# Kernel tuning notes

Hardware: AMD Instinct MI355X
Metric: run time of the kernel (lower is better)

Reference implementation:

```python
import jax, jax.numpy as jnp
import numpy as np

N_NODES = 200_000
N_EDGES = 6_400_000
N_GRAPHS = 512
F_IN = 92   # CGCNN atom feature dim
WIDTH = 10  # hard-coded config.width in GCNSimple
F_OUT = 1   # output_features


def setup_inputs() -> dict:
    key = jax.random.key(0)
    ks = jax.random.split(key, 10)
    atom_features = jax.random.normal(ks[0], (N_NODES, F_IN), dtype=jnp.float32)
    r = jax.random.normal(ks[1], (N_EDGES, 3), dtype=jnp.float32)
    W_emb = jax.random.normal(ks[2], (F_IN, WIDTH), dtype=jnp.float32) * 0.1
    b_emb = jax.random.normal(ks[3], (WIDTH,), dtype=jnp.float32) * 0.1
    W1 = jax.random.normal(ks[4], (WIDTH, WIDTH), dtype=jnp.float32) * 0.3
    b1 = jax.random.normal(ks[5], (WIDTH,), dtype=jnp.float32) * 0.1
    W2 = jax.random.normal(ks[6], (WIDTH, F_OUT), dtype=jnp.float32) * 0.3
    b2 = jax.random.normal(ks[7], (F_OUT,), dtype=jnp.float32) * 0.1
    src = jax.random.randint(ks[8], (N_EDGES,), 0, N_NODES, dtype=jnp.int32)
    dst = jax.random.randint(ks[9], (N_EDGES,), 0, N_NODES, dtype=jnp.int32)
    graph_ids = jnp.sort(jax.random.randint(jax.random.fold_in(key, 99), (N_NODES,), 0, N_GRAPHS, dtype=jnp.int32))
    return {
        "atom_features": atom_features, "r": r,
        "W_emb": W_emb, "b_emb": b_emb, "W1": W1, "b1": b1, "W2": W2, "b2": b2,
        "src": src, "dst": dst, "graph_ids": graph_ids, "num_graphs": N_GRAPHS,
    }


def reference(atom_features, r, W_emb, b_emb, W1, b1, W2, b2, src, dst, graph_ids, num_graphs):
    n = atom_features.shape[0]
    dt = atom_features.dtype
    # edge weights: exp(-||r||^2 / lengthscale^2), lengthscale = 1
    ew = jnp.exp(-jnp.sum(r * r, axis=1))  # [E]

    # unweighted degrees (DGL GraphConv norm='both' ignores edge_weight in norm)
    out_deg = jnp.clip(jnp.zeros(n, dt).at[src].add(1.0), 1.0)
    in_deg = jnp.clip(jnp.zeros(n, dt).at[dst].add(1.0), 1.0)
    inv_sqrt_out = out_deg ** -0.5
    inv_sqrt_in = in_deg ** -0.5

    def gconv(x, W, b, mm_first):
        # DGL GraphConv, norm='both': scale by src deg, weighted-sum aggregate,
        # scale by dst deg; weight applied before aggregation iff in > out.
        x = x * inv_sqrt_out[:, None]
        if mm_first:
            x = x @ W
        msg = x[src] * ew[:, None]                      # [E, d] gather
        agg = jax.ops.segment_sum(msg, dst, num_segments=n)  # [N, d] scatter-add
        if not mm_first:
            agg = agg @ W
        return agg * inv_sqrt_in[:, None] + b

    h = atom_features @ W_emb + b_emb                  # atom embedding [N, 10]
    x = jax.nn.relu(gconv(h, W1, b1, mm_first=False))  # 10 -> 10 (in == out: aggregate first)
    x = gconv(x, W2, b2, mm_first=True)                # 10 -> 1  (in > out: mm first)

    # AvgPooling: mean node feature per graph
    counts = jax.ops.segment_sum(jnp.ones(n, dt), graph_ids, num_segments=num_graphs)
    pooled = jax.ops.segment_sum(x, graph_ids, num_segments=num_graphs) / counts[:, None]
    return jnp.squeeze(pooled)  # [num_graphs]
```

## Files before the change

kernel.cpp:

```cpp
#include <hip/hip_runtime.h>
#include <math.h>

#define NNODES  200000
#define NEDGES  6400000
#define NGRAPHS 512
#define FIN     92
#define WID     10
#define HPAD    16
#define NBLK    ((NNODES + 255) / 256)

#define LBITS   10
#define LSIZE   1024
#define LMASK   (LSIZE - 1)
#define NB      196
#define PBLK    512
#define EPB     (NEDGES / PBLK)
#define TILE    2500
#define NTILE   (EPB / TILE)
#define CELLS   (2 * NB)
#define CNT_N   (CELLS * PBLK)
#define SBLKS   (CNT_N / 256)

#define CHBITS  14
#define NCHK    13
#define KEYS    (LSIZE * NCHK)
#define KPT     (KEYS / 256)

#define LPN     8
#define LPNSH   3
#define NPB     (256 / LPN)
#define AGG_BLKS (NNODES / NPB)

__global__ void k_part_count(const int* __restrict__ src,
                             const int* __restrict__ dst,
                             int* __restrict__ cnt) {
    __shared__ int hD[NB];
    __shared__ int hS[NB];
    int tid = threadIdx.x, k = blockIdx.x;
    if (tid < NB) { hD[tid] = 0; hS[tid] = 0; }
    __syncthreads();
    int base = k * EPB;
    for (int i = tid; i < EPB; i += 256) {
        int e = base + i;
        atomicAdd(&hD[dst[e] >> LBITS], 1);
        atomicAdd(&hS[src[e] >> LBITS], 1);
    }
    __syncthreads();
    if (tid < NB) {
        cnt[tid * PBLK + k] = hD[tid];
        cnt[(NB + tid) * PBLK + k] = hS[tid];
    }
}

__global__ void k_scan_partial(const int* __restrict__ cnt,
                               int* __restrict__ partial) {
    __shared__ int sdata[256];
    int tid = threadIdx.x;
    sdata[tid] = cnt[blockIdx.x * 256 + tid];
    __syncthreads();
    for (int s = 128; s > 0; s >>= 1) {
        if (tid < s) sdata[tid] += sdata[tid + s];
        __syncthreads();
    }
    if (tid == 0) partial[blockIdx.x] = sdata[0];
}

__global__ void k_scan_top(int* __restrict__ partial) {
    __shared__ int buf[1024];
    __shared__ int carry_s;
    if (threadIdx.x == 0) carry_s = 0;
    __syncthreads();
    for (int base = 0; base < SBLKS; base += 1024) {
        int i = base + threadIdx.x;
        int c = carry_s;
        int orig = (i < SBLKS) ? partial[i] : 0;
        buf[threadIdx.x] = orig;
        __syncthreads();
        for (int off = 1; off < 1024; off <<= 1) {
            int t = (threadIdx.x >= off) ? buf[threadIdx.x - off] : 0;
            __syncthreads();
            buf[threadIdx.x] += t;
            __syncthreads();
        }
        if (i < SBLKS) partial[i] = buf[threadIdx.x] - orig + c;
        __syncthreads();
        if (threadIdx.x == 0) carry_s = c + buf[1023];
        __syncthreads();
    }
}

__global__ void k_scan_apply(int* __restrict__ cnt,
                             const int* __restrict__ partial) {
    __shared__ int buf[256];
    int tid = threadIdx.x;
    int i = blockIdx.x * 256 + tid;
    int v = cnt[i];
    buf[tid] = v;
    __syncthreads();
    for (int off = 1; off < 256; off <<= 1) {
        int t = (tid >= off) ? buf[tid - off] : 0;
        __syncthreads();
        buf[tid] += t;
        __syncthreads();
    }
    cnt[i] = buf[tid] - v + partial[blockIdx.x];
}

__global__ void k_part_scatter(const float* __restrict__ r,
                               const int* __restrict__ src,
                               const int* __restrict__ dst,
                               const int* __restrict__ cnt,
                               float2* __restrict__ dstpart,
                               unsigned short* __restrict__ srcpart) {
    __shared__ int curD[NB], curS[NB];
    __shared__ int hD[NB], hS[NB];
    __shared__ int baseD[NB], baseS[NB];
    __shared__ int segD[NB], segS[NB];
    __shared__ int sbuf[256];
    __shared__ float2 stD[TILE];
    __shared__ int    ddD[TILE];
    __shared__ unsigned short stS[TILE];
    __shared__ int    ddS[TILE];

    int tid = threadIdx.x, k = blockIdx.x;
    if (tid < NB) {
        curD[tid] = cnt[tid * PBLK + k];
        curS[tid] = cnt[(NB + tid) * PBLK + k] - NEDGES;
    }
    __syncthreads();

    int base = k * EPB;
    for (int t = 0; t < NTILE; t++) {
        int tbase = base + t * TILE;
        if (tid < NB) { hD[tid] = 0; hS[tid] = 0; }
        __syncthreads();
        for (int i = tid; i < TILE; i += 256) {
            int e = tbase + i;
            atomicAdd(&hD[dst[e] >> LBITS], 1);
            atomicAdd(&hS[src[e] >> LBITS], 1);
        }
        __syncthreads();
        int v = (tid < NB) ? hD[tid] : 0;
        sbuf[tid] = v;
        __syncthreads();
        for (int off = 1; off < 256; off <<= 1) {
            int tv = (tid >= off) ? sbuf[tid - off] : 0;
            __syncthreads();
            sbuf[tid] += tv;
            __syncthreads();
        }
        if (tid < NB) { baseD[tid] = sbuf[tid] - v; segD[tid] = curD[tid]; }
        __syncthreads();
        int v2 = (tid < NB) ? hS[tid] : 0;
        sbuf[tid] = v2;
        __syncthreads();
        for (int off = 1; off < 256; off <<= 1) {
            int tv = (tid >= off) ? sbuf[tid - off] : 0;
            __syncthreads();
            sbuf[tid] += tv;
            __syncthreads();
        }
        if (tid < NB) {
            baseS[tid] = sbuf[tid] - v2;
            segS[tid] = curS[tid];
            curD[tid] += hD[tid];
            curS[tid] += hS[tid];
            hD[tid] = baseD[tid];
            hS[tid] = baseS[tid];
        }
        __syncthreads();
        for (int i = tid; i < TILE; i += 256) {
            int e = tbase + i;
            int s = src[e], d = dst[e];
            float x = r[3 * e + 0];
            float y = r[3 * e + 1];
            float z = r[3 * e + 2];
            float w = expf(-(x * x + y * y + z * z));
            int cd = d >> LBITS;
            int idx = atomicAdd(&hD[cd], 1);
            stD[idx] = make_float2(w, __int_as_float((s << LBITS) | (d & LMASK)));
            ddD[idx] = segD[cd] + (idx - baseD[cd]);
            int cs = s >> LBITS;
            int ids = atomicAdd(&hS[cs], 1);
            stS[ids] = (unsigned short)(s & LMASK);
            ddS[ids] = segS[cs] + (ids - baseS[cs]);
        }
        __syncthreads();
        for (int i = tid; i < TILE; i += 256) {
            dstpart[ddD[i]] = stD[i];
            srcpart[ddS[i]] = stS[i];
        }
        __syncthreads();
    }
}

__global__ void k_bucket_odeg(const unsigned short* __restrict__ srcpart,
                              const int* __restrict__ cnt,
                              float* __restrict__ inv_out) {
    __shared__ int hist[LSIZE];
    int tid = threadIdx.x, b = blockIdx.x;
    int bstart = cnt[(NB + b) * PBLK] - NEDGES;
    int bend = (b == NB - 1) ? NEDGES : (cnt[(NB + b + 1) * PBLK] - NEDGES);
    for (int l = tid; l < LSIZE; l += 256) hist[l] = 0;
    __syncthreads();
    for (int p = bstart + tid; p < bend; p += 256)
        atomicAdd(&hist[srcpart[p]], 1);
    __syncthreads();
    for (int l = tid; l < LSIZE; l += 256) {
        int n = (b << LBITS) + l;
        if (n < NNODES) {
            int c = hist[l];
            inv_out[n] = rsqrtf((float)(c < 1 ? 1 : c));
        }
    }
}

__global__ void k_bucket_csr(const float2* __restrict__ dstpart,
                             const int* __restrict__ cnt,
                             float2* __restrict__ csr,
                             int* __restrict__ row_ptr,
                             float* __restrict__ inv_in) {
    __shared__ int hist[KEYS];
    __shared__ int sbuf[256];
    int tid = threadIdx.x, b = blockIdx.x;
    int bstart = cnt[b * PBLK];
    int bend = cnt[(b + 1) * PBLK];

    for (int j = tid; j < KEYS; j += 256) hist[j] = 0;
    __syncthreads();
    for (int p = bstart + tid; p < bend; p += 256) {
        unsigned pk = __float_as_uint(dstpart[p].y);
        atomicAdd(&hist[(pk & LMASK) * NCHK + (pk >> 24)], 1);
    }
    __syncthreads();
    int kb = tid * KPT;
    int sum = 0;
    for (int j = 0; j < KPT; j++) sum += hist[kb + j];
    sbuf[tid] = sum;
    __syncthreads();
    for (int off = 1; off < 256; off <<= 1) {
        int tv = (tid >= off) ? sbuf[tid - off] : 0;
        __syncthreads();
        sbuf[tid] += tv;
        __syncthreads();
    }
    int run = sbuf[tid] - sum + bstart;
    for (int j = 0; j < KPT; j++) {
        int c = hist[kb + j];
        hist[kb + j] = run;
        run += c;
    }
    __syncthreads();
    for (int l = tid; l < LSIZE; l += 256) {
        int rs = hist[l * NCHK];
        int re = (l == LSIZE - 1) ? bend : hist[(l + 1) * NCHK];
        int n = (b << LBITS) + l;
        if (n < NNODES) {
            row_ptr[n] = rs;
            int c = re - rs;
            inv_in[n] = rsqrtf((float)(c < 1 ? 1 : c));
        }
    }
    __syncthreads();
    for (int p = bstart + tid; p < bend; p += 256) {
        float2 rec = dstpart[p];
        unsigned pk = __float_as_uint(rec.y);
        int pos = atomicAdd(&hist[(pk & LMASK) * NCHK + (pk >> 24)], 1);
        csr[pos] = make_float2(rec.x, __int_as_float((int)(pk >> LBITS)));
    }
}

__global__ void k_embed(const float* __restrict__ A,
                        const float* __restrict__ Wemb,
                        const float* __restrict__ bemb,
                        const float* __restrict__ inv_out,
                        float* __restrict__ hs) {
    __shared__ float sW[FIN * WID];
    __shared__ float sb[WID];
    for (int i = threadIdx.x; i < FIN * WID; i += blockDim.x) sW[i] = Wemb[i];
    if (threadIdx.x < WID) sb[threadIdx.x] = bemb[threadIdx.x];
    __syncthreads();

    int n = blockIdx.x * blockDim.x + threadIdx.x;
    if (n >= NNODES) return;

    float acc[WID];
#pragma unroll
    for (int k = 0; k < WID; k++) acc[k] = sb[k];

    const float4* row4 = reinterpret_cast<const float4*>(A + (size_t)n * FIN);
#pragma unroll
    for (int f4 = 0; f4 < FIN / 4; f4++) {
        float4 v = row4[f4];
        int f = f4 * 4;
#pragma unroll
        for (int k = 0; k < WID; k++) acc[k] += v.x * sW[(f + 0) * WID + k];
#pragma unroll
        for (int k = 0; k < WID; k++) acc[k] += v.y * sW[(f + 1) * WID + k];
#pragma unroll
        for (int k = 0; k < WID; k++) acc[k] += v.z * sW[(f + 2) * WID + k];
#pragma unroll
        for (int k = 0; k < WID; k++) acc[k] += v.w * sW[(f + 3) * WID + k];
    }

    float sc = inv_out[n];
    float* out = hs + (size_t)n * HPAD;
    float4 o0 = make_float4(acc[0] * sc, acc[1] * sc, acc[2] * sc, acc[3] * sc);
    float4 o1 = make_float4(acc[4] * sc, acc[5] * sc, acc[6] * sc, acc[7] * sc);
    float2 o2 = make_float2(acc[8] * sc, acc[9] * sc);
    *reinterpret_cast<float4*>(out + 0) = o0;
    *reinterpret_cast<float4*>(out + 4) = o1;
    *reinterpret_cast<float2*>(out + 8) = o2;
}

__global__ void k_agg1(const float2* __restrict__ csr,
                       const int* __restrict__ row_ptr,
                       const float* __restrict__ hs,
                       const float* __restrict__ W1,
                       const float* __restrict__ b1,
                       const float* __restrict__ W2,
                       const float* __restrict__ inv_in,
                       const float* __restrict__ inv_out,
                       float* __restrict__ sproj) {
    __shared__ float sW1[WID * WID];
    __shared__ float sb1[WID];
    __shared__ float sW2[WID];
    for (int i = threadIdx.x; i < WID * WID; i += blockDim.x) sW1[i] = W1[i];
    if (threadIdx.x < WID) {
        sb1[threadIdx.x] = b1[threadIdx.x];
        sW2[threadIdx.x] = W2[threadIdx.x];
    }
    __syncthreads();

    int tid = threadIdx.x;
    int sub = tid & (LPN - 1);
    int n = blockIdx.x * NPB + (tid >> LPNSH);

    int start = row_ptr[n];
    int end = (n == NNODES - 1) ? NEDGES : row_ptr[n + 1];

    float acc[WID];
#pragma unroll
    for (int k = 0; k < WID; k++) acc[k] = 0.0f;

    int p = start + sub;
    for (int c = 0; c < NCHK; c++) {
        int slim = (c + 1) << CHBITS;
        while (p < end) {
            float2 c2 = csr[p];
            int s = __float_as_int(c2.y);
            if (s >= slim) break;
            float w = c2.x;
            const float* hrow = hs + (size_t)s * HPAD;
            float4 a = *reinterpret_cast<const float4*>(hrow + 0);
            float4 b = *reinterpret_cast<const float4*>(hrow + 4);
            float2 cc = *reinterpret_cast<const float2*>(hrow + 8);
            acc[0] += w * a.x; acc[1] += w * a.y; acc[2] += w * a.z; acc[3] += w * a.w;
            acc[4] += w * b.x; acc[5] += w * b.y; acc[6] += w * b.z; acc[7] += w * b.w;
            acc[8] += w * cc.x; acc[9] += w * cc.y;
            p += LPN;
        }
        __syncthreads();
    }
    for (; p < end; p += LPN) {
        float2 c2 = csr[p];
        float w = c2.x;
        int s = __float_as_int(c2.y);
        const float* hrow = hs + (size_t)s * HPAD;
        float4 a = *reinterpret_cast<const float4*>(hrow + 0);
        float4 b = *reinterpret_cast<const float4*>(hrow + 4);
        float2 cc = *reinterpret_cast<const float2*>(hrow + 8);
        acc[0] += w * a.x; acc[1] += w * a.y; acc[2] += w * a.z; acc[3] += w * a.w;
        acc[4] += w * b.x; acc[5] += w * b.y; acc[6] += w * b.z; acc[7] += w * b.w;
        acc[8] += w * cc.x; acc[9] += w * cc.y;
    }

#pragma unroll
    for (int m = 1; m < LPN; m <<= 1) {
#pragma unroll
        for (int k = 0; k < WID; k++) acc[k] += __shfl_xor(acc[k], m, 64);
    }

    float ii = inv_in[n];
    float dot = 0.0f;
#pragma unroll
    for (int j = 0; j < WID; j++) {
        float y = 0.0f;
#pragma unroll
        for (int k = 0; k < WID; k++) y += acc[k] * sW1[k * WID + j];
        y = y * ii + sb1[j];
        y = y > 0.0f ? y : 0.0f;
        dot += y * sW2[j];
    }
    if (sub == 0) sproj[n] = dot * inv_out[n];
}

__global__ void k_agg2_pool(const float2* __restrict__ csr,
                            const int* __restrict__ row_ptr,
                            const float* __restrict__ sproj,
                            const float* __restrict__ inv_in,
                            const float* __restrict__ b2,
                            const int* __restrict__ graph_ids,
                            float* __restrict__ pooled) {
    int tid = threadIdx.x;
    int lane = tid & 63;
    int sub = tid & (LPN - 1);
    int n = blockIdx.x * NPB + (tid >> LPNSH);

    int start = row_ptr[n];
    int end = (n == NNODES - 1) ? NEDGES : row_ptr[n + 1];
    float sum = 0.0f;
    for (int p = start + sub; p < end; p += LPN) {
        float2 c2 = csr[p];
        sum += c2.x * sproj[__float_as_int(c2.y)];
    }
#pragma unroll
    for (int m = 1; m < LPN; m <<= 1) sum += __shfl_xor(sum, m, 64);

    float v = sum * inv_in[n] + b2[0];
    int g = graph_ids[n];

#pragma unroll
    for (int off = LPN; off < 64; off <<= 1) {
        float vv = __shfl_down(v, off, 64);
        int gg = __shfl_down(g, off, 64);
        if (lane + off < 64 && gg == g) v += vv;
    }
    int gprev = __shfl_up(g, LPN, 64);
    bool head = (sub == 0) && (lane < LPN || gprev != g);
    if (head) atomicAdd(&pooled[g], v);
}

__global__ void k_final(const float* __restrict__ pooled,
                        const int* __restrict__ gids,
                        float* __restrict__ out) {
    int g = blockIdx.x * blockDim.x + threadIdx.x;
    if (g >= NGRAPHS) return;
    int lo = 0, hi = NNODES;
    while (lo < hi) { int m = (lo + hi) >> 1; if (gids[m] < g) lo = m + 1; else hi = m; }
    int first = lo;
    hi = NNODES;
    while (lo < hi) { int m = (lo + hi) >> 1; if (gids[m] < g + 1) lo = m + 1; else hi = m; }
    int cnt = lo - first;
    out[g] = pooled[g] / (float)(cnt > 0 ? cnt : 1);
}

extern "C" void kernel_launch(void* const* d_in, const int* in_sizes, int n_in,
                              void* d_out, int out_size, void* d_ws, size_t ws_size,
                              hipStream_t stream) {
    const float* atom = (const float*)d_in[0];
    const float* r    = (const float*)d_in[1];
    const float* Wemb = (const float*)d_in[2];
    const float* bemb = (const float*)d_in[3];
    const float* W1   = (const float*)d_in[4];
    const float* b1   = (const float*)d_in[5];
    const float* W2   = (const float*)d_in[6];
    const float* b2   = (const float*)d_in[7];
    const int*   src  = (const int*)d_in[8];
    const int*   dst  = (const int*)d_in[9];
    const int*   gids = (const int*)d_in[10];
    float* out = (float*)d_out;

    char* w = (char*)d_ws;
    float* pooled  = (float*)w;  w += (size_t)NGRAPHS * 4;
    int*   cnt     = (int*)w;    w += (size_t)CNT_N * 4;
    int*   partial = (int*)w;    w += (size_t)((SBLKS + 3) & ~3) * 4;
    int*   row_ptr = (int*)w;    w += (size_t)((NNODES + 4) & ~3) * 4;
    float* inv_in  = (float*)w;  w += (size_t)NNODES * 4;
    float* inv_out = (float*)w;  w += (size_t)NNODES * 4;
    float* sproj   = (float*)w;  w += (size_t)NNODES * 4;
    float* hs      = (float*)w;  w += (size_t)NNODES * HPAD * 4;
    float2* dstpart = (float2*)w; w += (size_t)NEDGES * 8;
    float2* csr     = (float2*)w; w += (size_t)NEDGES * 8;
    unsigned short* srcpart = (unsigned short*)csr;

    hipMemsetAsync(pooled, 0, (size_t)NGRAPHS * 4, stream);

    const int B = 256;

    k_part_count<<<PBLK, B, 0, stream>>>(src, dst, cnt);
    k_scan_partial<<<SBLKS, B, 0, stream>>>(cnt, partial);
    k_scan_top<<<1, 1024, 0, stream>>>(partial);
    k_scan_apply<<<SBLKS, B, 0, stream>>>(cnt, partial);
    k_part_scatter<<<PBLK, B, 0, stream>>>(r, src, dst, cnt, dstpart, srcpart);
    k_bucket_odeg<<<NB, B, 0, stream>>>(srcpart, cnt, inv_out);
    k_bucket_csr<<<NB, B, 0, stream>>>(dstpart, cnt, csr, row_ptr, inv_in);
    k_embed<<<NBLK, B, 0, stream>>>(atom, Wemb, bemb, inv_out, hs);
    k_agg1<<<AGG_BLKS, B, 0, stream>>>(csr, row_ptr, hs, W1, b1, W2, inv_in, inv_out, sproj);
    k_agg2_pool<<<AGG_BLKS, B, 0, stream>>>(csr, row_ptr, sproj, inv_in, b2, gids, pooled);
    k_final<<<(NGRAPHS + B - 1) / B, B, 0, stream>>>(pooled, gids, out);
}
```

Measured before the change: 716.0 us.

## Split CSR bucket build into 128-node sub-buckets across 1600 blocks

```diff
diff --git a/kernel.cpp b/kernel.cpp
--- a/kernel.cpp
+++ b/kernel.cpp
@@ -23,8 +23,14 @@
 
 #define CHBITS  14
 #define NCHK    13
-#define KEYS    (LSIZE * NCHK)
-#define KPT     (KEYS / 256)
+
+#define NSUB    1563
+#define SUBW    1600
+#define SKEYS   (128 * NCHK)
+#define SKPAD   1792
+#define SKPT    7
+#define SMAX    5120
+#define CSR_GRID 1600
 
 #define LPN     8
 #define LPNSH   3
@@ -33,22 +39,35 @@
 
 __global__ void k_part_count(const int* __restrict__ src,
                              const int* __restrict__ dst,
-                             int* __restrict__ cnt) {
-    __shared__ int hD[NB];
+                             int* __restrict__ cnt,
+                             int* __restrict__ subcnt) {
+    __shared__ int hSub[NSUB];
     __shared__ int hS[NB];
     int tid = threadIdx.x, k = blockIdx.x;
-    if (tid < NB) { hD[tid] = 0; hS[tid] = 0; }
+    for (int i = tid; i < NSUB; i += 256) hSub[i] = 0;
+    if (tid < NB) hS[tid] = 0;
     __syncthreads();
     int base = k * EPB;
     for (int i = tid; i < EPB; i += 256) {
         int e = base + i;
-        atomicAdd(&hD[dst[e] >> LBITS], 1);
+        atomicAdd(&hSub[dst[e] >> 7], 1);
         atomicAdd(&hS[src[e] >> LBITS], 1);
     }
     __syncthreads();
     if (tid < NB) {
-        cnt[tid * PBLK + k] = hD[tid];
+        int s = 0;
+        int b0 = tid * 8;
+#pragma unroll
+        for (int j = 0; j < 8; j++) {
+            int ix = b0 + j;
+            if (ix < NSUB) s += hSub[ix];
+        }
+        cnt[tid * PBLK + k] = s;
         cnt[(NB + tid) * PBLK + k] = hS[tid];
+    }
+    for (int i = tid; i < NSUB; i += 256) {
+        int v = hSub[i];
+        if (v) atomicAdd(&subcnt[i], v);
     }
 }
 
@@ -104,6 +123,38 @@
         __syncthreads();
     }
     cnt[i] = buf[tid] - v + partial[blockIdx.x];
+}
+
+__global__ void k_subscan(int* __restrict__ subcnt) {
+    __shared__ int sbuf[256];
+    int tid = threadIdx.x;
+    int vals[SKPT];
+    int sum = 0;
+#pragma unroll
+    for (int j = 0; j < SKPT; j++) {
+        int c = tid * SKPT + j;
+        int v = (c < NSUB) ? subcnt[c] : 0;
+        vals[j] = v;
+        sum += v;
+    }
+    sbuf[tid] = sum;
+    __syncthreads();
+    for (int off = 1; off < 256; off <<= 1) {
+        int t = (tid >= off) ? sbuf[tid - off] : 0;
+        __syncthreads();
+        sbuf[tid] += t;
+        __syncthreads();
+    }
+    int run = sbuf[tid] - sum;
+#pragma unroll
+    for (int j = 0; j < SKPT; j++) {
+        int c = tid * SKPT + j;
+        if (c < NSUB) {
+            subcnt[c] = run;
+            run += vals[j];
+        }
+    }
+    if (tid == 0) subcnt[NSUB] = NEDGES;
 }
 
 __global__ void k_part_scatter(const float* __restrict__ r,
@@ -216,26 +267,38 @@
 }
 
 __global__ void k_bucket_csr(const float2* __restrict__ dstpart,
-                             const int* __restrict__ cnt,
+                             const int* __restrict__ subscan,
                              float2* __restrict__ csr,
                              int* __restrict__ row_ptr,
                              float* __restrict__ inv_in) {
-    __shared__ int hist[KEYS];
+    __shared__ int hist[SKPAD];
     __shared__ int sbuf[256];
-    int tid = threadIdx.x, b = blockIdx.x;
-    int bstart = cnt[b * PBLK];
-    int bend = cnt[(b + 1) * PBLK];
-
-    for (int j = tid; j < KEYS; j += 256) hist[j] = 0;
+    __shared__ float2 stout[SMAX];
+    int tid = threadIdx.x;
+    int q = blockIdx.x / 200;
+    int par = blockIdx.x % 200;
+    if (par >= NB) return;
+    int sub = par * 8 + q;
+    if (sub >= NSUB) return;
+    int bstart = subscan[par * 8];
+    int pe = par * 8 + 8;
+    int bend = subscan[pe > NSUB ? NSUB : pe];
+    int substart = subscan[sub];
+    int subend = subscan[sub + 1];
+    int sz = subend - substart;
+
+    for (int j = tid; j < SKPAD; j += 256) hist[j] = 0;
     __syncthreads();
     for (int p = bstart + tid; p < bend; p += 256) {
         unsigned pk = __float_as_uint(dstpart[p].y);
-        atomicAdd(&hist[(pk & LMASK) * NCHK + (pk >> 24)], 1);
-    }
-    __syncthreads();
-    int kb = tid * KPT;
+        if (((pk >> 7) & 7u) == (unsigned)q)
+            atomicAdd(&hist[(pk & 127u) * NCHK + (pk >> 24)], 1);
+    }
+    __syncthreads();
+    int kb = tid * SKPT;
     int sum = 0;
-    for (int j = 0; j < KPT; j++) sum += hist[kb + j];
+#pragma unroll
+    for (int j = 0; j < SKPT; j++) sum += hist[kb + j];
     sbuf[tid] = sum;
     __syncthreads();
     for (int off = 1; off < 256; off <<= 1) {
@@ -244,17 +307,19 @@
         sbuf[tid] += tv;
         __syncthreads();
     }
-    int run = sbuf[tid] - sum + bstart;
-    for (int j = 0; j < KPT; j++) {
+    int run = sbuf[tid] - sum + substart;
+#pragma unroll
+    for (int j = 0; j < SKPT; j++) {
         int c = hist[kb + j];
         hist[kb + j] = run;
         run += c;
     }
     __syncthreads();
-    for (int l = tid; l < LSIZE; l += 256) {
+    if (tid < 128) {
+        int l = tid;
         int rs = hist[l * NCHK];
-        int re = (l == LSIZE - 1) ? bend : hist[(l + 1) * NCHK];
-        int n = (b << LBITS) + l;
+        int re = (l == 127) ? subend : hist[(l + 1) * NCHK];
+        int n = (sub << 7) + l;
         if (n < NNODES) {
             row_ptr[n] = rs;
             int c = re - rs;
@@ -262,11 +327,25 @@
         }
     }
     __syncthreads();
-    for (int p = bstart + tid; p < bend; p += 256) {
-        float2 rec = dstpart[p];
-        unsigned pk = __float_as_uint(rec.y);
-        int pos = atomicAdd(&hist[(pk & LMASK) * NCHK + (pk >> 24)], 1);
-        csr[pos] = make_float2(rec.x, __int_as_float((int)(pk >> LBITS)));
+    if (sz <= SMAX) {
+        for (int p = bstart + tid; p < bend; p += 256) {
+            float2 rec = dstpart[p];
+            unsigned pk = __float_as_uint(rec.y);
+            if (((pk >> 7) & 7u) != (unsigned)q) continue;
+            int pos = atomicAdd(&hist[(pk & 127u) * NCHK + (pk >> 24)], 1);
+            stout[pos - substart] = make_float2(rec.x, __int_as_float((int)(pk >> LBITS)));
+        }
+        __syncthreads();
+        for (int i = tid; i < sz; i += 256)
+            csr[substart + i] = stout[i];
+    } else {
+        for (int p = bstart + tid; p < bend; p += 256) {
+            float2 rec = dstpart[p];
+            unsigned pk = __float_as_uint(rec.y);
+            if (((pk >> 7) & 7u) != (unsigned)q) continue;
+            int pos = atomicAdd(&hist[(pk & 127u) * NCHK + (pk >> 24)], 1);
+            csr[pos] = make_float2(rec.x, __int_as_float((int)(pk >> LBITS)));
+        }
     }
 }
 
@@ -463,6 +542,7 @@
 
     char* w = (char*)d_ws;
     float* pooled  = (float*)w;  w += (size_t)NGRAPHS * 4;
+    int*   subw    = (int*)w;    w += (size_t)SUBW * 4;
     int*   cnt     = (int*)w;    w += (size_t)CNT_N * 4;
     int*   partial = (int*)w;    w += (size_t)((SBLKS + 3) & ~3) * 4;
     int*   row_ptr = (int*)w;    w += (size_t)((NNODES + 4) & ~3) * 4;
@@ -475,16 +555,18 @@
     unsigned short* srcpart = (unsigned short*)csr;
 
     hipMemsetAsync(pooled, 0, (size_t)NGRAPHS * 4, stream);
+    hipMemsetAsync(subw, 0, (size_t)SUBW * 4, stream);
 
     const int B = 256;
 
-    k_part_count<<<PBLK, B, 0, stream>>>(src, dst, cnt);
+    k_part_count<<<PBLK, B, 0, stream>>>(src, dst, cnt, subw);
     k_scan_partial<<<SBLKS, B, 0, stream>>>(cnt, partial);
     k_scan_top<<<1, 1024, 0, stream>>>(partial);
     k_scan_apply<<<SBLKS, B, 0, stream>>>(cnt, partial);
+    k_subscan<<<1, B, 0, stream>>>(subw);
     k_part_scatter<<<PBLK, B, 0, stream>>>(r, src, dst, cnt, dstpart, srcpart);
     k_bucket_odeg<<<NB, B, 0, stream>>>(srcpart, cnt, inv_out);
-    k_bucket_csr<<<NB, B, 0, stream>>>(dstpart, cnt, csr, row_ptr, inv_in);
+    k_bucket_csr<<<CSR_GRID, B, 0, stream>>>(dstpart, subw, csr, row_ptr, inv_in);
     k_embed<<<NBLK, B, 0, stream>>>(atom, Wemb, bemb, inv_out, hs);
     k_agg1<<<AGG_BLKS, B, 0, stream>>>(csr, row_ptr, hs, W1, b1, W2, inv_in, inv_out, sproj);
     k_agg2_pool<<<AGG_BLKS, B, 0, stream>>>(csr, row_ptr, sproj, inv_in, b2, gids, pooled);
```

Result: slower. 847.3 us (+18.3%).

## Partition destinations into 128-node sub-buckets and stage CSR output in LDS

Applied to the files above, without the earlier changes.

```diff
diff --git a/kernel.cpp b/kernel.cpp
--- a/kernel.cpp
+++ b/kernel.cpp
@@ -13,18 +13,24 @@
 #define LSIZE   1024
 #define LMASK   (LSIZE - 1)
 #define NB      196
+#define SUBSH   7
+#define SUBN    128
+#define NSUB    1563
 #define PBLK    512
 #define EPB     (NEDGES / PBLK)
-#define TILE    2500
+#define TILE    1250
 #define NTILE   (EPB / TILE)
-#define CELLS   (2 * NB)
+#define CELLS   (NSUB + NB)
 #define CNT_N   (CELLS * PBLK)
 #define SBLKS   (CNT_N / 256)
+#define CPT     7
 
 #define CHBITS  14
 #define NCHK    13
-#define KEYS    (LSIZE * NCHK)
-#define KPT     (KEYS / 256)
+#define SKEYS   (SUBN * NCHK)
+#define SKPAD   1792
+#define SKPT    7
+#define SMAX    5120
 
 #define LPN     8
 #define LPNSH   3
@@ -34,22 +40,21 @@
 __global__ void k_part_count(const int* __restrict__ src,
                              const int* __restrict__ dst,
                              int* __restrict__ cnt) {
-    __shared__ int hD[NB];
+    __shared__ int hSub[NSUB];
     __shared__ int hS[NB];
     int tid = threadIdx.x, k = blockIdx.x;
-    if (tid < NB) { hD[tid] = 0; hS[tid] = 0; }
+    for (int i = tid; i < NSUB; i += 256) hSub[i] = 0;
+    if (tid < NB) hS[tid] = 0;
     __syncthreads();
     int base = k * EPB;
     for (int i = tid; i < EPB; i += 256) {
         int e = base + i;
-        atomicAdd(&hD[dst[e] >> LBITS], 1);
+        atomicAdd(&hSub[dst[e] >> SUBSH], 1);
         atomicAdd(&hS[src[e] >> LBITS], 1);
     }
     __syncthreads();
-    if (tid < NB) {
-        cnt[tid * PBLK + k] = hD[tid];
-        cnt[(NB + tid) * PBLK + k] = hS[tid];
-    }
+    for (int i = tid; i < NSUB; i += 256) cnt[i * PBLK + k] = hSub[i];
+    if (tid < NB) cnt[(NSUB + tid) * PBLK + k] = hS[tid];
 }
 
 __global__ void k_scan_partial(const int* __restrict__ cnt,
@@ -112,10 +117,8 @@
                                const int* __restrict__ cnt,
                                float2* __restrict__ dstpart,
                                unsigned short* __restrict__ srcpart) {
-    __shared__ int curD[NB], curS[NB];
-    __shared__ int hD[NB], hS[NB];
-    __shared__ int baseD[NB], baseS[NB];
-    __shared__ int segD[NB], segS[NB];
+    __shared__ int curD[NSUB], hD[NSUB], baseD[NSUB], segD[NSUB];
+    __shared__ int curS[NB], hS[NB], baseS[NB], segS[NB];
     __shared__ int sbuf[256];
     __shared__ float2 stD[TILE];
     __shared__ int    ddD[TILE];
@@ -123,25 +126,33 @@
     __shared__ int    ddS[TILE];
 
     int tid = threadIdx.x, k = blockIdx.x;
-    if (tid < NB) {
-        curD[tid] = cnt[tid * PBLK + k];
-        curS[tid] = cnt[(NB + tid) * PBLK + k] - NEDGES;
-    }
+    for (int i = tid; i < NSUB; i += 256) curD[i] = cnt[i * PBLK + k];
+    if (tid < NB) curS[tid] = cnt[(NSUB + tid) * PBLK + k] - NEDGES;
     __syncthreads();
 
     int base = k * EPB;
     for (int t = 0; t < NTILE; t++) {
         int tbase = base + t * TILE;
-        if (tid < NB) { hD[tid] = 0; hS[tid] = 0; }
+        for (int i = tid; i < NSUB; i += 256) hD[i] = 0;
+        if (tid < NB) hS[tid] = 0;
         __syncthreads();
         for (int i = tid; i < TILE; i += 256) {
             int e = tbase + i;
-            atomicAdd(&hD[dst[e] >> LBITS], 1);
+            atomicAdd(&hD[dst[e] >> SUBSH], 1);
             atomicAdd(&hS[src[e] >> LBITS], 1);
         }
         __syncthreads();
-        int v = (tid < NB) ? hD[tid] : 0;
-        sbuf[tid] = v;
+        int cb = tid * CPT;
+        int vals[CPT];
+        int sum = 0;
+#pragma unroll
+        for (int j = 0; j < CPT; j++) {
+            int c = cb + j;
+            int v = (c < NSUB) ? hD[c] : 0;
+            vals[j] = v;
+            sum += v;
+        }
+        sbuf[tid] = sum;
         __syncthreads();
         for (int off = 1; off < 256; off <<= 1) {
             int tv = (tid >= off) ? sbuf[tid - off] : 0;
@@ -149,7 +160,18 @@
             sbuf[tid] += tv;
             __syncthreads();
         }
-        if (tid < NB) { baseD[tid] = sbuf[tid] - v; segD[tid] = curD[tid]; }
+        int run = sbuf[tid] - sum;
+#pragma unroll
+        for (int j = 0; j < CPT; j++) {
+            int c = cb + j;
+            if (c < NSUB) {
+                baseD[c] = run;
+                segD[c] = curD[c];
+                curD[c] += vals[j];
+                hD[c] = run;
+                run += vals[j];
+            }
+        }
         __syncthreads();
         int v2 = (tid < NB) ? hS[tid] : 0;
         sbuf[tid] = v2;
@@ -163,9 +185,7 @@
         if (tid < NB) {
             baseS[tid] = sbuf[tid] - v2;
             segS[tid] = curS[tid];
-            curD[tid] += hD[tid];
-            curS[tid] += hS[tid];
-            hD[tid] = baseD[tid];
+            curS[tid] += v2;
             hS[tid] = baseS[tid];
         }
         __syncthreads();
@@ -176,7 +196,7 @@
             float y = r[3 * e + 1];
             float z = r[3 * e + 2];
             float w = expf(-(x * x + y * y + z * z));
-            int cd = d >> LBITS;
+            int cd = d >> SUBSH;
             int idx = atomicAdd(&hD[cd], 1);
             stD[idx] = make_float2(w, __int_as_float((s << LBITS) | (d & LMASK)));
             ddD[idx] = segD[cd] + (idx - baseD[cd]);
@@ -199,8 +219,8 @@
                               float* __restrict__ inv_out) {
     __shared__ int hist[LSIZE];
     int tid = threadIdx.x, b = blockIdx.x;
-    int bstart = cnt[(NB + b) * PBLK] - NEDGES;
-    int bend = (b == NB - 1) ? NEDGES : (cnt[(NB + b + 1) * PBLK] - NEDGES);
+    int bstart = cnt[(NSUB + b) * PBLK] - NEDGES;
+    int bend = (b == NB - 1) ? NEDGES : (cnt[(NSUB + b + 1) * PBLK] - NEDGES);
     for (int l = tid; l < LSIZE; l += 256) hist[l] = 0;
     __syncthreads();
     for (int p = bstart + tid; p < bend; p += 256)
@@ -220,22 +240,26 @@
                              float2* __restrict__ csr,
                              int* __restrict__ row_ptr,
                              float* __restrict__ inv_in) {
-    __shared__ int hist[KEYS];
+    __shared__ int hist[SKPAD];
     __shared__ int sbuf[256];
-    int tid = threadIdx.x, b = blockIdx.x;
-    int bstart = cnt[b * PBLK];
-    int bend = cnt[(b + 1) * PBLK];
-
-    for (int j = tid; j < KEYS; j += 256) hist[j] = 0;
-    __syncthreads();
-    for (int p = bstart + tid; p < bend; p += 256) {
+    __shared__ float2 stout[SMAX];
+    int tid = threadIdx.x;
+    int sub = blockIdx.x;
+    int substart = cnt[sub * PBLK];
+    int subend = cnt[(sub + 1) * PBLK];
+    int sz = subend - substart;
+
+    for (int j = tid; j < SKPAD; j += 256) hist[j] = 0;
+    __syncthreads();
+    for (int p = substart + tid; p < subend; p += 256) {
         unsigned pk = __float_as_uint(dstpart[p].y);
-        atomicAdd(&hist[(pk & LMASK) * NCHK + (pk >> 24)], 1);
-    }
-    __syncthreads();
-    int kb = tid * KPT;
+        atomicAdd(&hist[(pk & 127u) * NCHK + (pk >> 24)], 1);
+    }
+    __syncthreads();
+    int kb = tid * SKPT;
     int sum = 0;
-    for (int j = 0; j < KPT; j++) sum += hist[kb + j];
+#pragma unroll
+    for (int j = 0; j < SKPT; j++) sum += hist[kb + j];
     sbuf[tid] = sum;
     __syncthreads();
     for (int off = 1; off < 256; off <<= 1) {
@@ -244,17 +268,19 @@
         sbuf[tid] += tv;
         __syncthreads();
     }
-    int run = sbuf[tid] - sum + bstart;
-    for (int j = 0; j < KPT; j++) {
+    int run = sbuf[tid] - sum + substart;
+#pragma unroll
+    for (int j = 0; j < SKPT; j++) {
         int c = hist[kb + j];
         hist[kb + j] = run;
         run += c;
     }
     __syncthreads();
-    for (int l = tid; l < LSIZE; l += 256) {
+    if (tid < SUBN) {
+        int l = tid;
         int rs = hist[l * NCHK];
-        int re = (l == LSIZE - 1) ? bend : hist[(l + 1) * NCHK];
-        int n = (b << LBITS) + l;
+        int re = (l == SUBN - 1) ? subend : hist[(l + 1) * NCHK];
+        int n = (sub << SUBSH) + l;
         if (n < NNODES) {
             row_ptr[n] = rs;
             int c = re - rs;
@@ -262,11 +288,23 @@
         }
     }
     __syncthreads();
-    for (int p = bstart + tid; p < bend; p += 256) {
-        float2 rec = dstpart[p];
-        unsigned pk = __float_as_uint(rec.y);
-        int pos = atomicAdd(&hist[(pk & LMASK) * NCHK + (pk >> 24)], 1);
-        csr[pos] = make_float2(rec.x, __int_as_float((int)(pk >> LBITS)));
+    if (sz <= SMAX) {
+        for (int p = substart + tid; p < subend; p += 256) {
+            float2 rec = dstpart[p];
+            unsigned pk = __float_as_uint(rec.y);
+            int pos = atomicAdd(&hist[(pk & 127u) * NCHK + (pk >> 24)], 1);
+            stout[pos - substart] = make_float2(rec.x, __int_as_float((int)(pk >> LBITS)));
+        }
+        __syncthreads();
+        for (int i = tid; i < sz; i += 256)
+            csr[substart + i] = stout[i];
+    } else {
+        for (int p = substart + tid; p < subend; p += 256) {
+            float2 rec = dstpart[p];
+            unsigned pk = __float_as_uint(rec.y);
+            int pos = atomicAdd(&hist[(pk & 127u) * NCHK + (pk >> 24)], 1);
+            csr[pos] = make_float2(rec.x, __int_as_float((int)(pk >> LBITS)));
+        }
     }
 }
 
@@ -484,7 +522,7 @@
     k_scan_apply<<<SBLKS, B, 0, stream>>>(cnt, partial);
     k_part_scatter<<<PBLK, B, 0, stream>>>(r, src, dst, cnt, dstpart, srcpart);
     k_bucket_odeg<<<NB, B, 0, stream>>>(srcpart, cnt, inv_out);
-    k_bucket_csr<<<NB, B, 0, stream>>>(dstpart, cnt, csr, row_ptr, inv_in);
+    k_bucket_csr<<<NSUB, B, 0, stream>>>(dstpart, cnt, csr, row_ptr, inv_in);
     k_embed<<<NBLK, B, 0, stream>>>(atom, Wemb, bemb, inv_out, hs);
     k_agg1<<<AGG_BLKS, B, 0, stream>>>(csr, row_ptr, hs, W1, b1, W2, inv_in, inv_out, sproj);
     k_agg2_pool<<<AGG_BLKS, B, 0, stream>>>(csr, row_ptr, sproj, inv_in, b2, gids, pooled);
```

Result: no change. 714.9 us (-0.2%).
